# Kernel optimization log

Measured on AMD Instinct MI355X. Metric: run time of the kernel, lower is better.

## Reference

```python
import jax, jax.numpy as jnp
import numpy as np

H, D, KV, S, PAST, BS, NB = 32, 128, 8, 128, 8064, 128, 128
T = PAST + S          # total context = 8192
NBLK = T // BS        # logical blocks used = 64
NEG = jnp.float32(-1e30)


def setup_inputs() -> dict:
    key = jax.random.key(0)
    ks = jax.random.split(key, 6)
    q = jax.random.normal(ks[0], (1, H, S, D), jnp.float32)
    k = jax.random.normal(ks[1], (1, KV, S, D), jnp.float32)
    v = jax.random.normal(ks[2], (1, KV, S, D), jnp.float32)
    pk = jax.random.normal(ks[3], (NB, KV, BS, D), jnp.float32)
    pv = jax.random.normal(ks[4], (NB, KV, BS, D), jnp.float32)
    # block table: 64 logical blocks mapped to distinct physical blocks (paged indirection)
    bt = jax.random.permutation(ks[5], NB)[:NBLK].astype(jnp.int32)
    return dict(
        query_state=q, key_state=k, value_state=v,
        attn_mask=jnp.ones((1,), jnp.float32),  # unused: causal prefill path (use_attention_mask=False)
        past_key_state=pk, past_value_state=pv,
        seq_position=PAST,
        scale=jnp.float32(1.0 / np.sqrt(D)),
        block_tables=bt, block_size=BS,
    )


def reference(query_state, key_state, value_state, attn_mask,
              past_key_state, past_value_state, seq_position, scale,
              block_tables, block_size):
    # phase == 'prefill', use_attention_mask=False -> paged_causal_attn_prefill
    kvh = past_key_state.shape[1]
    s_new = query_state.shape[2]
    total = seq_position + s_new  # static python int

    # --- append new K/V into the paged cache at positions [seq_position, total) ---
    pos_new = seq_position + jnp.arange(s_new)
    blk = block_tables[pos_new // block_size]
    off = pos_new % block_size
    k_new = jnp.transpose(key_state[0], (1, 0, 2))    # [S, KV, D]
    v_new = jnp.transpose(value_state[0], (1, 0, 2))
    kc = past_key_state.at[blk, :, off, :].set(k_new)
    vc = past_value_state.at[blk, :, off, :].set(v_new)

    # --- gather the full context [0, total) through the block table ---
    pos = jnp.arange(total)
    blk_a = block_tables[pos // block_size]
    off_a = pos % block_size
    K = kc[blk_a, :, off_a, :]   # [T, KV, D]
    V = vc[blk_a, :, off_a, :]

    # --- grouped-query causal attention ---
    g = query_state.shape[1] // kvh
    q = query_state.reshape(kvh, g, s_new, -1)                 # [KV, G, S, D]
    scores = jnp.einsum('kgsd,tkd->kgst', q, K) * scale        # [KV, G, S, T]
    causal = pos[None, :] <= (seq_position + jnp.arange(s_new))[:, None]  # [S, T]
    scores = jnp.where(causal[None, None], scores, NEG)
    probs = jax.nn.softmax(scores, axis=-1)
    out = jnp.einsum('kgst,tkd->kgsd', probs, V)               # [KV, G, S, D]

    h = kvh * g
    out = out.reshape(1, h, s_new, -1)                         # [1, H, S, D]
    out = jnp.transpose(out, (0, 2, 1, 3)).reshape(1, s_new, h * out.shape[-1])
    return out
```

## Files before the change

### kernel.cpp

```cpp
#include <hip/hip_runtime.h>


typedef unsigned short u16;
typedef unsigned int u32;
typedef __bf16 bf16x8 __attribute__((ext_vector_type(8)));
typedef float f32x16 __attribute__((ext_vector_type(16)));
typedef float f32x4 __attribute__((ext_vector_type(4)));
typedef u32 u32x4 __attribute__((ext_vector_type(4)));
typedef u32 u32x2 __attribute__((ext_vector_type(2)));

#define NHEAD 32
#define DH 128
#define NKV 8
#define SQ 128
#define PAST_T 8064
#define TOTAL_T 8192
#define BK 32
#define KSTR 136
#define VSTR 36
#define WSPP (16384 + 256)

__device__ __forceinline__ u32 bf16rne(float f) {
  u32 u = __builtin_bit_cast(u32, f);
  return (u + 0x7FFFu + ((u >> 16) & 1u)) >> 16;
}
__device__ __forceinline__ u32 pk2(float lo, float hi) {
  return bf16rne(lo) | (bf16rne(hi) << 16);
}

template <int NPART>
__global__ __launch_bounds__(256, 2) void flash_part(
    const float* __restrict__ q, const float* __restrict__ knew,
    const float* __restrict__ vnew, const float* __restrict__ pk,
    const float* __restrict__ pv, const int* __restrict__ btab,
    const float* __restrict__ scp, float* __restrict__ ws) {
  constexpr int CHUNK = TOTAL_T / NPART;
  constexpr int NITER = CHUNK / BK;
  __shared__ __attribute__((aligned(16))) u16 k_s[2 * BK * KSTR];
  __shared__ __attribute__((aligned(16))) u16 vt_s[2 * DH * VSTR];
  __shared__ int bt_s[64];

  const int p = blockIdx.x, h = blockIdx.y, kv = h >> 2;
  const int tid = threadIdx.x;
  const int lane = tid & 63, w = tid >> 6;
  const int l31 = lane & 31, grp = lane >> 5;
  const int pstart = p * CHUNK;

  if (tid < 64) bt_s[tid] = btab[tid];
  const float scale = scp[0];

  u32x4 qf[8];
  {
    const float* qp = q + ((size_t)(h * SQ + w * 32 + l31)) * DH;
#pragma unroll
    for (int st = 0; st < 8; ++st) {
      const f32x4 a = *(const f32x4*)(qp + st * 16 + grp * 8);
      const f32x4 b = *(const f32x4*)(qp + st * 16 + grp * 8 + 4);
      u32x4 f;
      f[0] = pk2(a[0], a[1]);
      f[1] = pk2(a[2], a[3]);
      f[2] = pk2(b[0], b[1]);
      f[3] = pk2(b[2], b[3]);
      qf[st] = f;
    }
  }

  f32x16 oacc[4];
#pragma unroll
  for (int i = 0; i < 4; ++i)
#pragma unroll
    for (int r = 0; r < 16; ++r) oacc[i][r] = 0.0f;
  float m_run = -3.0e38f, l_run = 0.0f;

  __syncthreads();

  f32x4 kr[4];
  float vr[16];
  const int kc4 = (tid & 31) * 4;
  const int ktrow = tid >> 5;
  const int vd = tid & 127;
  const int vtseg = (tid >> 7) * 2;

  auto load_tile = [&](int it) {
    const int t0 = pstart + it * BK;
    const float *sk, *sv;
    if (t0 < PAST_T) {
      const size_t boff =
          (((size_t)bt_s[t0 >> 7] * NKV + kv) * 128 + (t0 & 127)) * (size_t)DH;
      sk = pk + boff;
      sv = pv + boff;
    } else {
      const size_t noff = ((size_t)kv * SQ + (t0 - PAST_T)) * (size_t)DH;
      sk = knew + noff;
      sv = vnew + noff;
    }
#pragma unroll
    for (int j = 0; j < 4; ++j)
      kr[j] = *(const f32x4*)(sk + (size_t)(j * 8 + ktrow) * DH + kc4);
#pragma unroll
    for (int rr = 0; rr < 8; ++rr) {
      const int t = vtseg + rr * 4;
      vr[2 * rr] = sv[(size_t)t * DH + vd];
      vr[2 * rr + 1] = sv[(size_t)(t + 1) * DH + vd];
    }
  };
  auto store_tile = [&](int buf) {
    u16* ks = k_s + buf * (BK * KSTR);
    u16* vs = vt_s + buf * (DH * VSTR);
#pragma unroll
    for (int j = 0; j < 4; ++j) {
      u32x2 pw;
      pw[0] = pk2(kr[j][0], kr[j][1]);
      pw[1] = pk2(kr[j][2], kr[j][3]);
      *(u32x2*)&ks[(j * 8 + ktrow) * KSTR + kc4] = pw;
    }
#pragma unroll
    for (int rr = 0; rr < 8; ++rr) {
      const int t = vtseg + rr * 4;
      *(u32*)&vs[vd * VSTR + t] = pk2(vr[2 * rr], vr[2 * rr + 1]);
    }
  };

  load_tile(0);
  store_tile(0);
  __syncthreads();

  for (int it = 0; it < NITER; ++it) {
    const int buf = it & 1;
    if (it + 1 < NITER) load_tile(it + 1);

    const u16* ks = k_s + buf * (BK * KSTR);
    const u16* vs = vt_s + buf * (DH * VSTR);
    const int t0 = pstart + it * BK;

    f32x16 sacc;
#pragma unroll
    for (int r = 0; r < 16; ++r) sacc[r] = 0.0f;
#pragma unroll
    for (int st = 0; st < 8; ++st) {
      const u32x4 kf = *(const u32x4*)&ks[l31 * KSTR + st * 16 + grp * 8];
      sacc = __builtin_amdgcn_mfma_f32_32x32x16_bf16(
          __builtin_bit_cast(bf16x8, kf), __builtin_bit_cast(bf16x8, qf[st]),
          sacc, 0, 0, 0);
    }

    const int qcol = w * 32 + l31;
    float sv_[16];
#pragma unroll
    for (int r = 0; r < 16; ++r) {
      const int trow = (r & 3) + 8 * (r >> 2) + 4 * grp;
      sv_[r] = ((t0 + trow - PAST_T) > qcol) ? -1.0e30f : sacc[r] * scale;
    }
    float rm = sv_[0];
#pragma unroll
    for (int r = 1; r < 16; ++r) rm = fmaxf(rm, sv_[r]);
    rm = fmaxf(rm, __shfl_xor(rm, 32, 64));
    const float m_new = fmaxf(m_run, rm);
    const float alpha = __expf(m_run - m_new);
    float pr[16], rs = 0.0f;
#pragma unroll
    for (int r = 0; r < 16; ++r) {
      pr[r] = __expf(sv_[r] - m_new);
      rs += pr[r];
    }
    rs += __shfl_xor(rs, 32, 64);
    l_run = l_run * alpha + rs;
    m_run = m_new;
#pragma unroll
    for (int i = 0; i < 4; ++i)
#pragma unroll
      for (int r = 0; r < 16; ++r) oacc[i][r] *= alpha;

    u32 pkk[8], xch[8];
#pragma unroll
    for (int j = 0; j < 8; ++j) pkk[j] = pk2(pr[2 * j], pr[2 * j + 1]);
#pragma unroll
    for (int j = 0; j < 8; ++j) xch[j] = (u32)__shfl_xor((int)pkk[j], 32, 64);

    u32x4 pf1, pf2;
    pf1[0] = grp ? xch[2] : pkk[0];
    pf1[1] = grp ? xch[3] : pkk[1];
    pf1[2] = grp ? pkk[2] : xch[0];
    pf1[3] = grp ? pkk[3] : xch[1];
    pf2[0] = grp ? xch[6] : pkk[4];
    pf2[1] = grp ? xch[7] : pkk[5];
    pf2[2] = grp ? pkk[6] : xch[4];
    pf2[3] = grp ? pkk[7] : xch[5];

#pragma unroll
    for (int dt = 0; dt < 4; ++dt) {
      const int dd = dt * 32 + l31;
      u32x2 a0 = *(const u32x2*)&vs[dd * VSTR + grp * 8];
      u32x2 a1 = *(const u32x2*)&vs[dd * VSTR + grp * 8 + 4];
      u32x4 av;
      av[0] = a0[0]; av[1] = a0[1]; av[2] = a1[0]; av[3] = a1[1];
      oacc[dt] = __builtin_amdgcn_mfma_f32_32x32x16_bf16(
          __builtin_bit_cast(bf16x8, av), __builtin_bit_cast(bf16x8, pf1),
          oacc[dt], 0, 0, 0);
      u32x2 b0 = *(const u32x2*)&vs[dd * VSTR + 16 + grp * 8];
      u32x2 b1 = *(const u32x2*)&vs[dd * VSTR + 16 + grp * 8 + 4];
      u32x4 bv;
      bv[0] = b0[0]; bv[1] = b0[1]; bv[2] = b1[0]; bv[3] = b1[1];
      oacc[dt] = __builtin_amdgcn_mfma_f32_32x32x16_bf16(
          __builtin_bit_cast(bf16x8, bv), __builtin_bit_cast(bf16x8, pf2),
          oacc[dt], 0, 0, 0);
    }

    if (it + 1 < NITER) store_tile(buf ^ 1);
    __syncthreads();
  }

  float* wsp = ws + (size_t)(h * NPART + p) * WSPP;
#pragma unroll
  for (int dt = 0; dt < 4; ++dt)
#pragma unroll
    for (int r = 0; r < 16; ++r) {
      const int dd = dt * 32 + (r & 3) + 8 * (r >> 2) + 4 * grp;
      wsp[dd * 128 + w * 32 + l31] = oacc[dt][r];
    }
  if (lane < 32) {
    wsp[16384 + w * 32 + lane] = m_run;
    wsp[16384 + 128 + w * 32 + lane] = l_run;
  }
}

template <int NPART>
__global__ __launch_bounds__(256, 2) void combine_out(
    const float* __restrict__ ws, float* __restrict__ out) {
  __shared__ float wgt_s[NPART][128];
  __shared__ float rden_s[128];
  __shared__ float tr_s[128 * 17];

  const int dblk = blockIdx.x;
  const int h = blockIdx.y;
  const int tid = threadIdx.x;
  const float* base = ws + (size_t)h * NPART * WSPP;

  if (tid < 128) {
    const int s = tid;
    float mv[NPART], M = -3.0e38f;
#pragma unroll
    for (int pp = 0; pp < NPART; ++pp) {
      mv[pp] = base[(size_t)pp * WSPP + 16384 + s];
      M = fmaxf(M, mv[pp]);
    }
    float denom = 0.0f;
#pragma unroll
    for (int pp = 0; pp < NPART; ++pp) {
      const float wv = __expf(mv[pp] - M);
      wgt_s[pp][s] = wv;
      denom += wv * base[(size_t)pp * WSPP + 16384 + 128 + s];
    }
    rden_s[s] = 1.0f / denom;
  }
  __syncthreads();

  const int sq = tid & 31, dr = tid >> 5;
#pragma unroll
  for (int rep = 0; rep < 2; ++rep) {
    const int dl = dr + 8 * rep;
    const int d = dblk * 16 + dl;
    float a[4] = {0.0f, 0.0f, 0.0f, 0.0f};
#pragma unroll
    for (int pp = 0; pp < NPART; ++pp) {
      const f32x4 o = *(const f32x4*)&base[(size_t)pp * WSPP + d * 128 + sq * 4];
#pragma unroll
      for (int j = 0; j < 4; ++j) a[j] += wgt_s[pp][sq * 4 + j] * o[j];
    }
#pragma unroll
    for (int j = 0; j < 4; ++j)
      tr_s[(sq * 4 + j) * 17 + dl] = a[j] * rden_s[sq * 4 + j];
  }
  __syncthreads();

#pragma unroll
  for (int rep = 0; rep < 2; ++rep) {
    const int s = (tid >> 2) + 64 * rep;
    const int dl0 = (tid & 3) * 4;
    f32x4 o;
#pragma unroll
    for (int j = 0; j < 4; ++j) o[j] = tr_s[s * 17 + dl0 + j];
    *(f32x4*)(out + (size_t)s * (NHEAD * DH) + h * DH + dblk * 16 + dl0) = o;
  }
}

extern "C" void kernel_launch(void* const* d_in, const int* in_sizes, int n_in,
                              void* d_out, int out_size, void* d_ws,
                              size_t ws_size, hipStream_t stream) {
  const float* q = (const float*)d_in[0];
  const float* knew = (const float*)d_in[1];
  const float* vnew = (const float*)d_in[2];
  const float* pk = (const float*)d_in[4];
  const float* pv = (const float*)d_in[5];
  const float* scp = (const float*)d_in[7];
  const int* btab = (const int*)d_in[8];
  float* ws = (float*)d_ws;
  float* out = (float*)d_out;

  const size_t need16 = (size_t)NHEAD * 16 * WSPP * sizeof(float);
  const size_t need8 = (size_t)NHEAD * 8 * WSPP * sizeof(float);
  if (ws_size >= need16) {
    flash_part<16><<<dim3(16, NHEAD), 256, 0, stream>>>(q, knew, vnew, pk, pv,
                                                        btab, scp, ws);
    combine_out<16><<<dim3(8, NHEAD), 256, 0, stream>>>(ws, out);
  } else if (ws_size >= need8) {
    flash_part<8><<<dim3(8, NHEAD), 256, 0, stream>>>(q, knew, vnew, pk, pv,
                                                      btab, scp, ws);
    combine_out<8><<<dim3(8, NHEAD), 256, 0, stream>>>(ws, out);
  }
}
```

Before: 180.8 us.

## Remap blocks for XCD KV locality, vectorize V loads, skip mask off-diagonal

Flattens the flash grid and remaps block IDs so blocks sharing a KV head and partition land together, aiming for better L2 reuse of K/V across the four grouped query heads. V tile loads become float4 vector loads with a transposed scatter into LDS using a new stride. The causal mask is applied only on tiles near the diagonal. The bf16 conversion now uses the HIP intrinsic, and the combine kernel runs twice as many blocks with half the work each. The new LDS stride and scalar reads may add bank conflicts or extra LDS instructions.

```diff
diff --git a/kernel.cpp b/kernel.cpp
--- a/kernel.cpp
+++ b/kernel.cpp
@@ -1,4 +1,5 @@
 #include <hip/hip_runtime.h>
+#include <hip/hip_bf16.h>
 
 
 typedef unsigned short u16;
@@ -17,15 +18,16 @@
 #define TOTAL_T 8192
 #define BK 32
 #define KSTR 136
-#define VSTR 36
+#define VSTR 34
 #define WSPP (16384 + 256)
 
-__device__ __forceinline__ u32 bf16rne(float f) {
-  u32 u = __builtin_bit_cast(u32, f);
-  return (u + 0x7FFFu + ((u >> 16) & 1u)) >> 16;
-}
-__device__ __forceinline__ u32 pk2(float lo, float hi) {
-  return bf16rne(lo) | (bf16rne(hi) << 16);
+__device__ __forceinline__ u32 pk2f(float lo, float hi) {
+  union {
+    __hip_bfloat162 b;
+    u32 u;
+  } cv;
+  cv.b = __float22bfloat162_rn(make_float2(lo, hi));
+  return cv.u;
 }
 
 template <int NPART>
@@ -40,7 +42,14 @@
   __shared__ __attribute__((aligned(16))) u16 vt_s[2 * DH * VSTR];
   __shared__ int bt_s[64];
 
-  const int p = blockIdx.x, h = blockIdx.y, kv = h >> 2;
+  const int bid = blockIdx.x;
+  const int r = bid & 31, u = bid >> 5;
+  const int g = r >> 3;
+  const int idx = u * 8 + (r & 7);
+  const int kv = idx & 7;
+  const int p = idx >> 3;
+  const int h = kv * 4 + g;
+
   const int tid = threadIdx.x;
   const int lane = tid & 63, w = tid >> 6;
   const int l31 = lane & 31, grp = lane >> 5;
@@ -57,10 +66,10 @@
       const f32x4 a = *(const f32x4*)(qp + st * 16 + grp * 8);
       const f32x4 b = *(const f32x4*)(qp + st * 16 + grp * 8 + 4);
       u32x4 f;
-      f[0] = pk2(a[0], a[1]);
-      f[1] = pk2(a[2], a[3]);
-      f[2] = pk2(b[0], b[1]);
-      f[3] = pk2(b[2], b[3]);
+      f[0] = pk2f(a[0], a[1]);
+      f[1] = pk2f(a[2], a[3]);
+      f[2] = pk2f(b[0], b[1]);
+      f[3] = pk2f(b[2], b[3]);
       qf[st] = f;
     }
   }
@@ -69,17 +78,17 @@
 #pragma unroll
   for (int i = 0; i < 4; ++i)
 #pragma unroll
-    for (int r = 0; r < 16; ++r) oacc[i][r] = 0.0f;
+    for (int rr = 0; rr < 16; ++rr) oacc[i][rr] = 0.0f;
   float m_run = -3.0e38f, l_run = 0.0f;
 
   __syncthreads();
 
   f32x4 kr[4];
-  float vr[16];
+  f32x4 v0[2], v1[2];
   const int kc4 = (tid & 31) * 4;
   const int ktrow = tid >> 5;
-  const int vd = tid & 127;
-  const int vtseg = (tid >> 7) * 2;
+  const int va4 = (tid & 31) * 4;
+  const int vtp = tid >> 5;
 
   auto load_tile = [&](int it) {
     const int t0 = pstart + it * BK;
@@ -98,10 +107,10 @@
     for (int j = 0; j < 4; ++j)
       kr[j] = *(const f32x4*)(sk + (size_t)(j * 8 + ktrow) * DH + kc4);
 #pragma unroll
-    for (int rr = 0; rr < 8; ++rr) {
-      const int t = vtseg + rr * 4;
-      vr[2 * rr] = sv[(size_t)t * DH + vd];
-      vr[2 * rr + 1] = sv[(size_t)(t + 1) * DH + vd];
+    for (int rr = 0; rr < 2; ++rr) {
+      const int t = 2 * (vtp + rr * 8);
+      v0[rr] = *(const f32x4*)(sv + (size_t)t * DH + va4);
+      v1[rr] = *(const f32x4*)(sv + (size_t)(t + 1) * DH + va4);
     }
   };
   auto store_tile = [&](int buf) {
@@ -110,14 +119,16 @@
 #pragma unroll
     for (int j = 0; j < 4; ++j) {
       u32x2 pw;
-      pw[0] = pk2(kr[j][0], kr[j][1]);
-      pw[1] = pk2(kr[j][2], kr[j][3]);
+      pw[0] = pk2f(kr[j][0], kr[j][1]);
+      pw[1] = pk2f(kr[j][2], kr[j][3]);
       *(u32x2*)&ks[(j * 8 + ktrow) * KSTR + kc4] = pw;
     }
 #pragma unroll
-    for (int rr = 0; rr < 8; ++rr) {
-      const int t = vtseg + rr * 4;
-      *(u32*)&vs[vd * VSTR + t] = pk2(vr[2 * rr], vr[2 * rr + 1]);
+    for (int rr = 0; rr < 2; ++rr) {
+      const int t = 2 * (vtp + rr * 8);
+#pragma unroll
+      for (int j = 0; j < 4; ++j)
+        *(u32*)&vs[(va4 + j) * VSTR + t] = pk2f(v0[rr][j], v1[rr][j]);
     }
   };
 
@@ -135,7 +146,7 @@
 
     f32x16 sacc;
 #pragma unroll
-    for (int r = 0; r < 16; ++r) sacc[r] = 0.0f;
+    for (int rr = 0; rr < 16; ++rr) sacc[rr] = 0.0f;
 #pragma unroll
     for (int st = 0; st < 8; ++st) {
       const u32x4 kf = *(const u32x4*)&ks[l31 * KSTR + st * 16 + grp * 8];
@@ -146,22 +157,27 @@
 
     const int qcol = w * 32 + l31;
     float sv_[16];
-#pragma unroll
-    for (int r = 0; r < 16; ++r) {
-      const int trow = (r & 3) + 8 * (r >> 2) + 4 * grp;
-      sv_[r] = ((t0 + trow - PAST_T) > qcol) ? -1.0e30f : sacc[r] * scale;
+    if (t0 > PAST_T - BK) {
+#pragma unroll
+      for (int rr = 0; rr < 16; ++rr) {
+        const int trow = (rr & 3) + 8 * (rr >> 2) + 4 * grp;
+        sv_[rr] = ((t0 + trow - PAST_T) > qcol) ? -1.0e30f : sacc[rr] * scale;
+      }
+    } else {
+#pragma unroll
+      for (int rr = 0; rr < 16; ++rr) sv_[rr] = sacc[rr] * scale;
     }
     float rm = sv_[0];
 #pragma unroll
-    for (int r = 1; r < 16; ++r) rm = fmaxf(rm, sv_[r]);
+    for (int rr = 1; rr < 16; ++rr) rm = fmaxf(rm, sv_[rr]);
     rm = fmaxf(rm, __shfl_xor(rm, 32, 64));
     const float m_new = fmaxf(m_run, rm);
     const float alpha = __expf(m_run - m_new);
     float pr[16], rs = 0.0f;
 #pragma unroll
-    for (int r = 0; r < 16; ++r) {
-      pr[r] = __expf(sv_[r] - m_new);
-      rs += pr[r];
+    for (int rr = 0; rr < 16; ++rr) {
+      pr[rr] = __expf(sv_[rr] - m_new);
+      rs += pr[rr];
     }
     rs += __shfl_xor(rs, 32, 64);
     l_run = l_run * alpha + rs;
@@ -169,11 +185,11 @@
 #pragma unroll
     for (int i = 0; i < 4; ++i)
 #pragma unroll
-      for (int r = 0; r < 16; ++r) oacc[i][r] *= alpha;
+      for (int rr = 0; rr < 16; ++rr) oacc[i][rr] *= alpha;
 
     u32 pkk[8], xch[8];
 #pragma unroll
-    for (int j = 0; j < 8; ++j) pkk[j] = pk2(pr[2 * j], pr[2 * j + 1]);
+    for (int j = 0; j < 8; ++j) pkk[j] = pk2f(pr[2 * j], pr[2 * j + 1]);
 #pragma unroll
     for (int j = 0; j < 8; ++j) xch[j] = (u32)__shfl_xor((int)pkk[j], 32, 64);
 
@@ -190,17 +206,21 @@
 #pragma unroll
     for (int dt = 0; dt < 4; ++dt) {
       const int dd = dt * 32 + l31;
-      u32x2 a0 = *(const u32x2*)&vs[dd * VSTR + grp * 8];
-      u32x2 a1 = *(const u32x2*)&vs[dd * VSTR + grp * 8 + 4];
+      const u16* vp = &vs[dd * VSTR + grp * 8];
       u32x4 av;
-      av[0] = a0[0]; av[1] = a0[1]; av[2] = a1[0]; av[3] = a1[1];
+      av[0] = *(const u32*)(vp + 0);
+      av[1] = *(const u32*)(vp + 2);
+      av[2] = *(const u32*)(vp + 4);
+      av[3] = *(const u32*)(vp + 6);
       oacc[dt] = __builtin_amdgcn_mfma_f32_32x32x16_bf16(
           __builtin_bit_cast(bf16x8, av), __builtin_bit_cast(bf16x8, pf1),
           oacc[dt], 0, 0, 0);
-      u32x2 b0 = *(const u32x2*)&vs[dd * VSTR + 16 + grp * 8];
-      u32x2 b1 = *(const u32x2*)&vs[dd * VSTR + 16 + grp * 8 + 4];
+      const u16* vq = vp + 16;
       u32x4 bv;
-      bv[0] = b0[0]; bv[1] = b0[1]; bv[2] = b1[0]; bv[3] = b1[1];
+      bv[0] = *(const u32*)(vq + 0);
+      bv[1] = *(const u32*)(vq + 2);
+      bv[2] = *(const u32*)(vq + 4);
+      bv[3] = *(const u32*)(vq + 6);
       oacc[dt] = __builtin_amdgcn_mfma_f32_32x32x16_bf16(
           __builtin_bit_cast(bf16x8, bv), __builtin_bit_cast(bf16x8, pf2),
           oacc[dt], 0, 0, 0);
@@ -214,9 +234,9 @@
 #pragma unroll
   for (int dt = 0; dt < 4; ++dt)
 #pragma unroll
-    for (int r = 0; r < 16; ++r) {
-      const int dd = dt * 32 + (r & 3) + 8 * (r >> 2) + 4 * grp;
-      wsp[dd * 128 + w * 32 + l31] = oacc[dt][r];
+    for (int rr = 0; rr < 16; ++rr) {
+      const int dd = dt * 32 + (rr & 3) + 8 * (rr >> 2) + 4 * grp;
+      wsp[dd * 128 + w * 32 + l31] = oacc[dt][rr];
     }
   if (lane < 32) {
     wsp[16384 + w * 32 + lane] = m_run;
@@ -229,7 +249,7 @@
     const float* __restrict__ ws, float* __restrict__ out) {
   __shared__ float wgt_s[NPART][128];
   __shared__ float rden_s[128];
-  __shared__ float tr_s[128 * 17];
+  __shared__ float tr_s[128 * 9];
 
   const int dblk = blockIdx.x;
   const int h = blockIdx.y;
@@ -256,10 +276,8 @@
   __syncthreads();
 
   const int sq = tid & 31, dr = tid >> 5;
-#pragma unroll
-  for (int rep = 0; rep < 2; ++rep) {
-    const int dl = dr + 8 * rep;
-    const int d = dblk * 16 + dl;
+  {
+    const int d = dblk * 8 + dr;
     float a[4] = {0.0f, 0.0f, 0.0f, 0.0f};
 #pragma unroll
     for (int pp = 0; pp < NPART; ++pp) {
@@ -269,18 +287,16 @@
     }
 #pragma unroll
     for (int j = 0; j < 4; ++j)
-      tr_s[(sq * 4 + j) * 17 + dl] = a[j] * rden_s[sq * 4 + j];
+      tr_s[(sq * 4 + j) * 9 + dr] = a[j] * rden_s[sq * 4 + j];
   }
   __syncthreads();
 
-#pragma unroll
-  for (int rep = 0; rep < 2; ++rep) {
-    const int s = (tid >> 2) + 64 * rep;
-    const int dl0 = (tid & 3) * 4;
+  {
+    const int s = tid >> 1, dl0 = (tid & 1) * 4;
     f32x4 o;
 #pragma unroll
-    for (int j = 0; j < 4; ++j) o[j] = tr_s[s * 17 + dl0 + j];
-    *(f32x4*)(out + (size_t)s * (NHEAD * DH) + h * DH + dblk * 16 + dl0) = o;
+    for (int j = 0; j < 4; ++j) o[j] = tr_s[s * 9 + dl0 + j];
+    *(f32x4*)(out + (size_t)s * (NHEAD * DH) + h * DH + dblk * 8 + dl0) = o;
   }
 }
 
@@ -300,12 +316,12 @@
   const size_t need16 = (size_t)NHEAD * 16 * WSPP * sizeof(float);
   const size_t need8 = (size_t)NHEAD * 8 * WSPP * sizeof(float);
   if (ws_size >= need16) {
-    flash_part<16><<<dim3(16, NHEAD), 256, 0, stream>>>(q, knew, vnew, pk, pv,
-                                                        btab, scp, ws);
-    combine_out<16><<<dim3(8, NHEAD), 256, 0, stream>>>(ws, out);
+    flash_part<16><<<dim3(32 * 16), 256, 0, stream>>>(q, knew, vnew, pk, pv,
+                                                      btab, scp, ws);
+    combine_out<16><<<dim3(16, NHEAD), 256, 0, stream>>>(ws, out);
   } else if (ws_size >= need8) {
-    flash_part<8><<<dim3(8, NHEAD), 256, 0, stream>>>(q, knew, vnew, pk, pv,
-                                                      btab, scp, ws);
-    combine_out<8><<<dim3(8, NHEAD), 256, 0, stream>>>(ws, out);
+    flash_part<8><<<dim3(32 * 8), 256, 0, stream>>>(q, knew, vnew, pk, pv,
+                                                    btab, scp, ws);
+    combine_out<8><<<dim3(16, NHEAD), 256, 0, stream>>>(ws, out);
   }
 }
```

New measurement: 176.3 us. -2.5%, faster.
